# Kernel tuning notes

Hardware: AMD Instinct MI355X
Metric: run time of the kernel (lower is better)

Reference implementation:

```python
import jax, jax.numpy as jnp
import numpy as np
from jax import lax

B, N, D_PTS = 8, 4096, 6
N_POINTS, N_SAMPLES, RADIUS = 1024, 32, 0.2
MLPS = [64, 64, 128]
BN_EPS = 1e-3  # keras BatchNormalization default epsilon


def safe_norm(diff, axis):
    # euclidean norm with a backward-safe sqrt (same forward values)
    sq = jnp.sum(diff * diff, axis=axis)
    pos = sq > 0
    return jnp.where(pos, jnp.sqrt(jnp.where(pos, sq, 1.0)), 0.0)


def setup_inputs() -> dict:
    key = jax.random.key(0)
    ks = jax.random.split(key, 2)
    xyz = jax.random.normal(ks[0], (B, N, 3), jnp.float32)
    points = jax.random.normal(ks[1], (B, N, D_PTS), jnp.float32)
    inp = {"xyz": xyz, "points": points}
    c_in = 3 + D_PTS
    for i, c_out in enumerate(MLPS):
        kw = jax.random.fold_in(key, 100 + i)
        inp[f"w{i}"] = jax.random.normal(kw, (c_in, c_out), jnp.float32) * (1.0 / np.sqrt(c_in))
        inp[f"b{i}"] = jnp.zeros((c_out,), jnp.float32)
        inp[f"g{i}"] = jnp.ones((c_out,), jnp.float32)
        inp[f"be{i}"] = jnp.zeros((c_out,), jnp.float32)
        c_in = c_out
    return inp


def fps(xyz, n_points):
    # farthest point sampling; original seeds with a random index, we use 0 deterministically
    b, n, _ = xyz.shape
    init_idx = jnp.zeros((b,), jnp.int32)
    mask0 = jnp.ones((b, n), xyz.dtype)
    def step(carry, _):
        mask, last = carry
        added = jnp.take_along_axis(xyz, last[:, None, None], axis=1)  # [B,1,D]
        dist = safe_norm(xyz - added, 2) * mask                        # [B,N]
        nxt = jnp.argmax(dist, axis=1).astype(jnp.int32)
        new_mask = jnp.minimum(dist * mask * 1e11, mask)
        return (new_mask, nxt), nxt
    _, ids = lax.scan(step, (mask0, init_idx), None, length=n_points - 1)
    return jnp.concatenate([init_idx[:, None], ids.T], axis=1)  # [B, n_points]


def gather_points(x, idx):
    # x: [B,N,C]; idx: [B,...] -> [B,...,C]
    b = x.shape[0]
    flat = idx.reshape(b, -1)
    out = jnp.take_along_axis(x, flat[..., None], axis=1)
    return out.reshape(idx.shape + (x.shape[-1],))


def query_ball(radius, n_samples, xyz, cent_xyz):
    # faithful to source: compares norm to radius**2 (source quirk), full argsort then slice
    diff = xyz[:, None, :, :] - cent_xyz[:, :, None, :]   # [B,n,N,3]
    dist = safe_norm(diff, 3)                              # [B,n,N]
    dist = jnp.minimum(dist, radius * radius)
    return jnp.argsort(dist, axis=2)[:, :, :n_samples]     # [B,n,n_samples]


def mlp_layer(h, w, b, g, be):
    # pointwise Dense + BatchNormalization (batch stats, axis=-1) + relu
    h = jnp.einsum('bnsc,cd->bnsd', h, w) + b
    mean = jnp.mean(h, axis=(0, 1, 2), keepdims=True)
    var = jnp.var(h, axis=(0, 1, 2), keepdims=True)
    h = g * (h - mean) * lax.rsqrt(var + BN_EPS) + be
    return jax.nn.relu(h)


def forward(xyz, points, params):
    cent_idx = fps(xyz, N_POINTS)                 # [B, n_points]
    cent_xyz = gather_points(xyz, cent_idx)       # [B, n_points, 3]
    group_idx = query_ball(RADIUS, N_SAMPLES, xyz, cent_xyz)  # [B, n_points, n_samples]
    group_xyz = gather_points(xyz, group_idx)     # [B, n_points, n_samples, 3]
    group_pts = gather_points(points, group_idx)  # [B, n_points, n_samples, D]
    h = jnp.concatenate([group_xyz, group_pts], axis=-1)
    for (w, b, g, be) in params:
        h = mlp_layer(h, w, b, g, be)
    return cent_xyz, jnp.max(h, axis=2)           # [B,n_points,3], [B,n_points,128]


def reference(xyz, points, w0, b0, g0, be0, w1, b1, g1, be1, w2, b2, g2, be2):
    params = [(w0, b0, g0, be0), (w1, b1, g1, be1), (w2, b2, g2, be2)]
    return forward(xyz, points, params)
```

## Files before the change

kernel.cpp:

```cpp
#include <hip/hip_runtime.h>

#define NPTS  4096
#define NB    8
#define NC    1024
#define NSAMP 32
#define DP    6
#define C0    9
#define C3    128
#define ROWS_TOT 262144

#define OFF_SS   (32ull<<10)
#define OFF_H0   (1ull<<20)
#define OFF_Y0   (16ull<<20)
#define OFF_Y1   (96ull<<20)
#define OFF_PSUM (168ull<<20)
#define OFF_PSQ  (172ull<<20)
#define OFF_GMX  (176ull<<20)
#define OFF_GMN  (180ull<<20)

typedef unsigned long long ull;

__device__ __forceinline__ float sqdist_noc(float x, float y, float z,
                                            float cx, float cy, float cz) {
  #pragma clang fp contract(off)
  float dx = x - cx, dy = y - cy, dz = z - cz;
  return dx * dx + dy * dy + dz * dz;
}

template <int CTRL, int RM>
__device__ __forceinline__ float dpp_mov_f(float x) {
  int xi = __float_as_int(x);
  int r = __builtin_amdgcn_update_dpp(xi, xi, CTRL, RM, 0xf, false);
  return __int_as_float(r);
}

__device__ __forceinline__ float wave64_fmax(float x) {
  x = fmaxf(x, dpp_mov_f<0x111, 0xf>(x));
  x = fmaxf(x, dpp_mov_f<0x112, 0xf>(x));
  x = fmaxf(x, dpp_mov_f<0x114, 0xf>(x));
  x = fmaxf(x, dpp_mov_f<0x118, 0xf>(x));
  x = fmaxf(x, dpp_mov_f<0x142, 0xa>(x));
  x = fmaxf(x, dpp_mov_f<0x143, 0xc>(x));
  return x;
}

__global__ __launch_bounds__(256)
void fps_kernel(const float* __restrict__ xyz, float* __restrict__ cent) {
  const int b = blockIdx.x;
  const int t = threadIdx.x;
  const float* X = xyz + (size_t)b * NPTS * 3;
  float* OC = cent + (size_t)b * NC * 3;

  __shared__ float4 sxyz[NPTS];
  __shared__ float4 wkc[2][4];
  __shared__ alignas(16) int wki[2][4];
  __shared__ int sidx[NC];

  for (int p = t; p < NPTS; p += 256)
    sxyz[p] = make_float4(X[p * 3 + 0], X[p * 3 + 1], X[p * 3 + 2], 0.f);
  __syncthreads();

  float px[16], py[16], pz[16], h[16];
  #pragma unroll
  for (int i = 0; i < 16; i++) {
    float4 v = sxyz[t * 16 + i];
    px[i] = v.x; py[i] = v.y; pz[i] = v.z;
    h[i] = fmaf(v.x, v.x, fmaf(v.y, v.y, v.z * v.z));
  }

  const int wv = t >> 6;
  float4 c;

  auto step_body = [&](int pw_) {
    const float c2x = c.x + c.x, c2y = c.y + c.y, c2z = c.z + c.z;
    float key[16]; int idx[16];
    #pragma unroll
    for (int i = 0; i < 16; i++) {
      key[i] = fmaf(pz[i], -c2z, fmaf(py[i], -c2y, fmaf(px[i], -c2x, h[i])));
      idx[i] = i;
    }
    #pragma unroll
    for (int s = 1; s < 16; s <<= 1) {
      #pragma unroll
      for (int i = 0; i < 16; i += 2 * s) {
        bool tk = key[i + s] > key[i];
        key[i] = tk ? key[i + s] : key[i];
        idx[i] = tk ? idx[i + s] : idx[i];
      }
    }
    const float mx = key[0];
    const int mj = idx[0];
    float4 cand = sxyz[(t << 4) + mj];
    float wm = wave64_fmax(mx);
    float smax = __int_as_float(__builtin_amdgcn_readlane(__float_as_int(wm), 63));
    if (mx == smax) {
      wkc[pw_][wv] = make_float4(cand.x, cand.y, cand.z, smax);
      wki[pw_][wv] = (t << 4) + mj;
    }
  };

  auto fold = [&](int pr_) -> int {
    float4 q0 = wkc[pr_][0], q1 = wkc[pr_][1];
    float4 q2 = wkc[pr_][2], q3 = wkc[pr_][3];
    const int4 ii = *(const int4*)&wki[pr_][0];
    bool g1 = q1.w > q0.w; float4 ca = g1 ? q1 : q0; int ia = g1 ? ii.y : ii.x;
    bool g3 = q3.w > q2.w; float4 cb = g3 ? q3 : q2; int ib = g3 ? ii.w : ii.z;
    bool gb = cb.w > ca.w; c = gb ? cb : ca; return gb ? ib : ia;
  };

  if (t == 0) { sidx[0] = 0; h[0] = -__builtin_inff(); }
  c = sxyz[0];
  step_body(1);
  __syncthreads();

  for (int k = 2; k < NC; k++) {
    const int pr = (k - 1) & 1, pw = k & 1;
    int gidx = fold(pr);
    if (t == 0) sidx[k - 1] = gidx;
    if ((gidx >> 4) == t) {
      int m = gidx & 15;
      #pragma unroll
      for (int i = 0; i < 16; i++)
        if (i == m) h[i] = -__builtin_inff();
    }
    step_body(pw);
    __syncthreads();
  }
  {
    int gidx = fold(1023 & 1);
    if (t == 0) sidx[NC - 1] = gidx;
  }
  __syncthreads();
  for (int i = t; i < NC; i += 256) {
    float4 cc = sxyz[sidx[i]];
    OC[i * 3 + 0] = cc.x;
    OC[i * 3 + 1] = cc.y;
    OC[i * 3 + 2] = cc.z;
  }
}

#define BCAP 256
__global__ __launch_bounds__(256)
void ball_kernel(const float* __restrict__ xyz, const float* __restrict__ pts,
                 const float* __restrict__ cent, float* __restrict__ h0) {
  const int blk = blockIdx.x;
  const int b = blk >> 10;
  const int t = threadIdx.x;
  const float* X = xyz + (size_t)b * NPTS * 3;
  const float* P = pts + (size_t)b * NPTS * DP;
  const float cx = cent[(size_t)blk * 3 + 0];
  const float cy = cent[(size_t)blk * 3 + 1];
  const float cz = cent[(size_t)blk * 3 + 2];

  __shared__ int scount;
  __shared__ ull skeys[BCAP];
  __shared__ ull ssorted[BCAP];
  __shared__ int sel[NSAMP];
  if (t == 0) scount = 0;
  __syncthreads();

  #pragma unroll
  for (int i = 0; i < 16; i++) {
    int j = t * 16 + i;
    float sq = sqdist_noc(X[j * 3 + 0], X[j * 3 + 1], X[j * 3 + 2], cx, cy, cz);
    if (sq < 0.0017f) {
      float d = (sq > 0.f) ? sqrtf(sq) : 0.f;
      if (d < 0.04f) {
        int pos = atomicAdd(&scount, 1);
        if (pos < BCAP)
          skeys[pos] = ((ull)(unsigned)__float_as_int(d) << 12) | (unsigned)j;
      }
    }
  }
  __syncthreads();
  const int M = min(scount, BCAP);

  if (t < M) {
    ull my = skeys[t];
    int r = 0;
    for (int j2 = 0; j2 < M; j2++) r += (skeys[j2] < my);
    ssorted[r] = my;
  }
  __syncthreads();

  if (t < NSAMP) {
    int v;
    if (t < M) {
      v = (int)(ssorted[t] & 0xFFFull);
    } else {
      int s = t - M;
      int idx = s;
      for (int it = 0; it < 40; it++) {
        int c = 0;
        for (int j2 = 0; j2 < M; j2++) c += ((int)(skeys[j2] & 0xFFFull) <= idx);
        int nidx = s + c;
        if (nidx == idx) break;
        idx = nidx;
      }
      v = idx;
    }
    sel[t] = v;
  }
  __syncthreads();

  float* H = h0 + (size_t)blk * NSAMP * C0;
  for (int e = t; e < NSAMP * C0; e += 256) {
    int k = e / C0;
    int c = e - k * C0;
    int j = sel[k];
    H[e] = (c < 3) ? X[j * 3 + c] : P[j * DP + (c - 3)];
  }
}

__global__ __launch_bounds__(256)
void dense0_kernel(const float* __restrict__ h0, const float* __restrict__ W,
                   const float* __restrict__ bias, float* __restrict__ yout,
                   float* __restrict__ psum, float* __restrict__ psq) {
  __shared__ float xs[64 * C0];
  __shared__ float ws[C0 * 64];
  __shared__ float red[2][16][64];
  const int blk = blockIdx.x, t = threadIdx.x;
  const size_t rbase = (size_t)blk * 64;
  for (int e = t; e < 64 * C0; e += 256) xs[e] = h0[rbase * C0 + e];
  for (int e = t; e < C0 * 64; e += 256) ws[e] = W[e];
  __syncthreads();
  const int rg = t >> 4, cg = t & 15;
  float acc[4][4];
  float4 bv = *(const float4*)(bias + cg * 4);
  #pragma unroll
  for (int r = 0; r < 4; r++) { acc[r][0] = bv.x; acc[r][1] = bv.y; acc[r][2] = bv.z; acc[r][3] = bv.w; }
  #pragma unroll
  for (int k = 0; k < C0; k++) {
    float4 wv = *(const float4*)(ws + k * 64 + cg * 4);
    #pragma unroll
    for (int r = 0; r < 4; r++) {
      float x = xs[(rg * 4 + r) * C0 + k];
      acc[r][0] = fmaf(x, wv.x, acc[r][0]);
      acc[r][1] = fmaf(x, wv.y, acc[r][1]);
      acc[r][2] = fmaf(x, wv.z, acc[r][2]);
      acc[r][3] = fmaf(x, wv.w, acc[r][3]);
    }
  }
  #pragma unroll
  for (int r = 0; r < 4; r++)
    *(float4*)(yout + (rbase + rg * 4 + r) * 64 + cg * 4) =
        make_float4(acc[r][0], acc[r][1], acc[r][2], acc[r][3]);
  #pragma unroll
  for (int c4 = 0; c4 < 4; c4++) {
    float s = 0.f, q = 0.f;
    #pragma unroll
    for (int r = 0; r < 4; r++) { float v = acc[r][c4]; s += v; q = fmaf(v, v, q); }
    red[0][rg][cg * 4 + c4] = s;
    red[1][rg][cg * 4 + c4] = q;
  }
  __syncthreads();
  if (t < 64) {
    float S = 0.f, Q = 0.f;
    #pragma unroll
    for (int g = 0; g < 16; g++) { S += red[0][g][t]; Q += red[1][g][t]; }
    psum[(size_t)t * 4096 + blk] = S;
    psq [(size_t)t * 4096 + blk] = Q;
  }
}

template <int RPB, int COUT, int CGN, int NBLKS, bool MM>
__global__ __launch_bounds__(256)
void dense_mid_kernel(const float* __restrict__ yin, const float* __restrict__ ssin,
                      const float* __restrict__ W, const float* __restrict__ bias,
                      float* __restrict__ yout,
                      float* __restrict__ psum, float* __restrict__ psq,
                      float* __restrict__ gmax, float* __restrict__ gmin) {
  constexpr int NG = 256 / CGN;
  __shared__ float xs[RPB * 68];
  __shared__ float ws[64 * COUT];
  __shared__ float scs[64], shs[64];
  __shared__ float red[2][NG][COUT];
  __shared__ float redm[MM ? 2 : 1][MM ? NG : 1][MM ? COUT : 1];
  const int blk = blockIdx.x, t = threadIdx.x;
  if (t < 64) { scs[t] = ssin[t]; shs[t] = ssin[128 + t]; }
  __syncthreads();
  const size_t rbase = (size_t)blk * RPB;
  for (int e = t; e < RPB * 64; e += 256) {
    int c = e & 63;
    float v = yin[rbase * 64 + e];
    xs[(e >> 6) * 68 + c] = fmaxf(fmaf(v, scs[c], shs[c]), 0.f);
  }
  for (int e = t; e < 64 * COUT; e += 256) ws[e] = W[e];
  __syncthreads();
  const int rg = t / CGN, cg = t % CGN;
  float acc[4][4];
  float4 bv = *(const float4*)(bias + cg * 4);
  #pragma unroll
  for (int r = 0; r < 4; r++) { acc[r][0] = bv.x; acc[r][1] = bv.y; acc[r][2] = bv.z; acc[r][3] = bv.w; }
  for (int k0 = 0; k0 < 64; k0 += 4) {
    float4 xv[4];
    #pragma unroll
    for (int r = 0; r < 4; r++)
      xv[r] = *(const float4*)(xs + (rg * 4 + r) * 68 + k0);
    #pragma unroll
    for (int kk = 0; kk < 4; kk++) {
      float4 wv = *(const float4*)(ws + (k0 + kk) * COUT + cg * 4);
      #pragma unroll
      for (int r = 0; r < 4; r++) {
        float x = (&xv[r].x)[kk];
        acc[r][0] = fmaf(x, wv.x, acc[r][0]);
        acc[r][1] = fmaf(x, wv.y, acc[r][1]);
        acc[r][2] = fmaf(x, wv.z, acc[r][2]);
        acc[r][3] = fmaf(x, wv.w, acc[r][3]);
      }
    }
  }
  if constexpr (!MM) {
    #pragma unroll
    for (int r = 0; r < 4; r++)
      *(float4*)(yout + (rbase + rg * 4 + r) * COUT + cg * 4) =
          make_float4(acc[r][0], acc[r][1], acc[r][2], acc[r][3]);
  }
  #pragma unroll
  for (int c4 = 0; c4 < 4; c4++) {
    float s = 0.f, q = 0.f;
    #pragma unroll
    for (int r = 0; r < 4; r++) { float v = acc[r][c4]; s += v; q = fmaf(v, v, q); }
    red[0][rg][cg * 4 + c4] = s;
    red[1][rg][cg * 4 + c4] = q;
    if constexpr (MM) {
      float mx = acc[0][c4], mn = acc[0][c4];
      #pragma unroll
      for (int r = 1; r < 4; r++) { mx = fmaxf(mx, acc[r][c4]); mn = fminf(mn, acc[r][c4]); }
      redm[0][rg][cg * 4 + c4] = mx;
      redm[1][rg][cg * 4 + c4] = mn;
    }
  }
  __syncthreads();
  if (t < COUT) {
    float S = 0.f, Q = 0.f;
    #pragma unroll
    for (int g = 0; g < NG; g++) { S += red[0][g][t]; Q += red[1][g][t]; }
    psum[(size_t)t * NBLKS + blk] = S;
    psq [(size_t)t * NBLKS + blk] = Q;
    if constexpr (MM) {
      float mx = redm[0][0][t], mn = redm[1][0][t];
      #pragma unroll
      for (int g = 1; g < NG; g++) { mx = fmaxf(mx, redm[0][g][t]); mn = fminf(mn, redm[1][g][t]); }
      gmax[(size_t)blk * COUT + t] = mx;
      gmin[(size_t)blk * COUT + t] = mn;
    }
  }
}

template <int NBLK>
__global__ __launch_bounds__(256)
void stats_final_kernel(const float* __restrict__ psum, const float* __restrict__ psq,
                        const float* __restrict__ g, const float* __restrict__ be,
                        float* __restrict__ ss_out) {
  const int c = blockIdx.x, t = threadIdx.x;
  float S = 0.f, Q = 0.f;
  for (int i = t; i < NBLK; i += 256) {
    S += psum[(size_t)c * NBLK + i];
    Q += psq [(size_t)c * NBLK + i];
  }
  __shared__ float sS[256], sQ[256];
  sS[t] = S; sQ[t] = Q;
  __syncthreads();
  #pragma unroll
  for (int off = 128; off; off >>= 1) {
    if (t < off) { sS[t] += sS[t + off]; sQ[t] += sQ[t + off]; }
    __syncthreads();
  }
  if (t == 0) {
    const float inv = 1.0f / 262144.0f;
    float mean = sS[0] * inv;
    float var = sQ[0] * inv - mean * mean;
    float scale = g[c] / sqrtf(var + 1e-3f);
    ss_out[c] = scale;
    ss_out[128 + c] = be[c] - mean * scale;
  }
}

__global__ __launch_bounds__(128)
void pool_final_kernel(const float* __restrict__ gmax, const float* __restrict__ gmin,
                       const float* __restrict__ ss2, float* __restrict__ out1) {
  const int blk = blockIdx.x, c = threadIdx.x;
  const float sc = ss2[c], sh = ss2[128 + c];
  float v = (sc >= 0.f) ? gmax[(size_t)blk * C3 + c] : gmin[(size_t)blk * C3 + c];
  out1[(size_t)blk * C3 + c] = fmaxf(fmaf(v, sc, sh), 0.f);
}

extern "C" void kernel_launch(void* const* d_in, const int* in_sizes, int n_in,
                              void* d_out, int out_size, void* d_ws, size_t ws_size,
                              hipStream_t stream) {
  const float* xyz = (const float*)d_in[0];
  const float* pts = (const float*)d_in[1];
  const float* w0 = (const float*)d_in[2];
  const float* b0 = (const float*)d_in[3];
  const float* g0 = (const float*)d_in[4];
  const float* be0 = (const float*)d_in[5];
  const float* w1 = (const float*)d_in[6];
  const float* b1 = (const float*)d_in[7];
  const float* g1 = (const float*)d_in[8];
  const float* be1 = (const float*)d_in[9];
  const float* w2 = (const float*)d_in[10];
  const float* b2 = (const float*)d_in[11];
  const float* g2 = (const float*)d_in[12];
  const float* be2 = (const float*)d_in[13];

  float* out = (float*)d_out;
  float* cent = out;
  float* out1 = out + (size_t)NB * NC * 3;

  char* ws = (char*)d_ws;
  float* ssA  = (float*)(ws + OFF_SS);
  float* h0   = (float*)(ws + OFF_H0);
  float* y0   = (float*)(ws + OFF_Y0);
  float* y1   = (float*)(ws + OFF_Y1);
  float* psum = (float*)(ws + OFF_PSUM);
  float* psq  = (float*)(ws + OFF_PSQ);
  float* gmx  = (float*)(ws + OFF_GMX);
  float* gmn  = (float*)(ws + OFF_GMN);

  fps_kernel<<<dim3(NB), dim3(256), 0, stream>>>(xyz, cent);
  ball_kernel<<<dim3(NB * NC), dim3(256), 0, stream>>>(xyz, pts, cent, h0);

  dense0_kernel<<<dim3(ROWS_TOT / 64), dim3(256), 0, stream>>>(h0, w0, b0, y0, psum, psq);
  stats_final_kernel<4096><<<dim3(64), dim3(256), 0, stream>>>(psum, psq, g0, be0, ssA + 0 * 256);

  dense_mid_kernel<64, 64, 16, 4096, false><<<dim3(ROWS_TOT / 64), dim3(256), 0, stream>>>(
      y0, ssA + 0 * 256, w1, b1, y1, psum, psq, nullptr, nullptr);
  stats_final_kernel<4096><<<dim3(64), dim3(256), 0, stream>>>(psum, psq, g1, be1, ssA + 1 * 256);

  dense_mid_kernel<32, 128, 32, 8192, true><<<dim3(ROWS_TOT / 32), dim3(256), 0, stream>>>(
      y1, ssA + 1 * 256, w2, b2, nullptr, psum, psq, gmx, gmn);
  stats_final_kernel<8192><<<dim3(128), dim3(256), 0, stream>>>(psum, psq, g2, be2, ssA + 2 * 256);

  pool_final_kernel<<<dim3(NB * NC), dim3(128), 0, stream>>>(gmx, gmn, ssA + 2 * 256, out1);

  (void)in_sizes; (void)n_in; (void)out_size; (void)ws_size;
}
```

Baseline: 885.3 us.

## Recompute MLP layers from h0 instead of storing intermediates; pack two FPS batches per block

The dense stages no longer write the 64-channel activations y0 and y1 to global memory. Each batch-norm statistics pass recomputes the earlier layers from the small 9-channel h0 buffer, which removes large global writes and reads at the cost of redundant FLOPs. FPS now runs two batches per 512-thread block, halving the number of blocks for the serial sampling loop. The two halves share __syncthreads, so each one waits on the other.

```diff
diff --git a/kernel.cpp b/kernel.cpp
--- a/kernel.cpp
+++ b/kernel.cpp
@@ -11,8 +11,6 @@
 
 #define OFF_SS   (32ull<<10)
 #define OFF_H0   (1ull<<20)
-#define OFF_Y0   (16ull<<20)
-#define OFF_Y1   (96ull<<20)
 #define OFF_PSUM (168ull<<20)
 #define OFF_PSQ  (172ull<<20)
 #define OFF_GMX  (176ull<<20)
@@ -44,26 +42,27 @@
   return x;
 }
 
-__global__ __launch_bounds__(256)
+__global__ __launch_bounds__(512)
 void fps_kernel(const float* __restrict__ xyz, float* __restrict__ cent) {
-  const int b = blockIdx.x;
-  const int t = threadIdx.x;
+  const int half = threadIdx.x >> 8;
+  const int t = threadIdx.x & 255;
+  const int b = blockIdx.x * 2 + half;
   const float* X = xyz + (size_t)b * NPTS * 3;
   float* OC = cent + (size_t)b * NC * 3;
 
-  __shared__ float4 sxyz[NPTS];
-  __shared__ float4 wkc[2][4];
-  __shared__ alignas(16) int wki[2][4];
-  __shared__ int sidx[NC];
+  __shared__ float4 sxyz[2][NPTS];
+  __shared__ float4 wkc[2][2][4];
+  __shared__ alignas(16) int wki[2][2][4];
+  __shared__ int sidx[2][NC];
 
   for (int p = t; p < NPTS; p += 256)
-    sxyz[p] = make_float4(X[p * 3 + 0], X[p * 3 + 1], X[p * 3 + 2], 0.f);
+    sxyz[half][p] = make_float4(X[p * 3 + 0], X[p * 3 + 1], X[p * 3 + 2], 0.f);
   __syncthreads();
 
   float px[16], py[16], pz[16], h[16];
   #pragma unroll
   for (int i = 0; i < 16; i++) {
-    float4 v = sxyz[t * 16 + i];
+    float4 v = sxyz[half][t * 16 + i];
     px[i] = v.x; py[i] = v.y; pz[i] = v.z;
     h[i] = fmaf(v.x, v.x, fmaf(v.y, v.y, v.z * v.z));
   }
@@ -90,33 +89,34 @@
     }
     const float mx = key[0];
     const int mj = idx[0];
-    float4 cand = sxyz[(t << 4) + mj];
+    float4 cand = sxyz[half][(t << 4) + mj];
     float wm = wave64_fmax(mx);
     float smax = __int_as_float(__builtin_amdgcn_readlane(__float_as_int(wm), 63));
     if (mx == smax) {
-      wkc[pw_][wv] = make_float4(cand.x, cand.y, cand.z, smax);
-      wki[pw_][wv] = (t << 4) + mj;
+      wkc[half][pw_][wv] = make_float4(cand.x, cand.y, cand.z, smax);
+      wki[half][pw_][wv] = (t << 4) + mj;
     }
   };
 
   auto fold = [&](int pr_) -> int {
-    float4 q0 = wkc[pr_][0], q1 = wkc[pr_][1];
-    float4 q2 = wkc[pr_][2], q3 = wkc[pr_][3];
-    const int4 ii = *(const int4*)&wki[pr_][0];
+    float4 q0 = wkc[half][pr_][0], q1 = wkc[half][pr_][1];
+    float4 q2 = wkc[half][pr_][2], q3 = wkc[half][pr_][3];
+    const int4 ii = *(const int4*)&wki[half][pr_][0];
     bool g1 = q1.w > q0.w; float4 ca = g1 ? q1 : q0; int ia = g1 ? ii.y : ii.x;
     bool g3 = q3.w > q2.w; float4 cb = g3 ? q3 : q2; int ib = g3 ? ii.w : ii.z;
     bool gb = cb.w > ca.w; c = gb ? cb : ca; return gb ? ib : ia;
   };
 
-  if (t == 0) { sidx[0] = 0; h[0] = -__builtin_inff(); }
-  c = sxyz[0];
+  if (t == 0) { sidx[half][0] = 0; }
+  if (t == 0) { h[0] = -__builtin_inff(); }
+  c = sxyz[half][0];
   step_body(1);
   __syncthreads();
 
   for (int k = 2; k < NC; k++) {
     const int pr = (k - 1) & 1, pw = k & 1;
     int gidx = fold(pr);
-    if (t == 0) sidx[k - 1] = gidx;
+    if (t == 0) sidx[half][k - 1] = gidx;
     if ((gidx >> 4) == t) {
       int m = gidx & 15;
       #pragma unroll
@@ -128,11 +128,11 @@
   }
   {
     int gidx = fold(1023 & 1);
-    if (t == 0) sidx[NC - 1] = gidx;
+    if (t == 0) sidx[half][NC - 1] = gidx;
   }
   __syncthreads();
   for (int i = t; i < NC; i += 256) {
-    float4 cc = sxyz[sidx[i]];
+    float4 cc = sxyz[half][sidx[half][i]];
     OC[i * 3 + 0] = cc.x;
     OC[i * 3 + 1] = cc.y;
     OC[i * 3 + 2] = cc.z;
@@ -213,9 +213,9 @@
 }
 
 __global__ __launch_bounds__(256)
-void dense0_kernel(const float* __restrict__ h0, const float* __restrict__ W,
-                   const float* __restrict__ bias, float* __restrict__ yout,
-                   float* __restrict__ psum, float* __restrict__ psq) {
+void pass0_kernel(const float* __restrict__ h0, const float* __restrict__ W,
+                  const float* __restrict__ bias,
+                  float* __restrict__ psum, float* __restrict__ psq) {
   __shared__ float xs[64 * C0];
   __shared__ float ws[C0 * 64];
   __shared__ float red[2][16][64];
@@ -242,10 +242,6 @@
     }
   }
   #pragma unroll
-  for (int r = 0; r < 4; r++)
-    *(float4*)(yout + (rbase + rg * 4 + r) * 64 + cg * 4) =
-        make_float4(acc[r][0], acc[r][1], acc[r][2], acc[r][3]);
-  #pragma unroll
   for (int c4 = 0; c4 < 4; c4++) {
     float s = 0.f, q = 0.f;
     #pragma unroll
@@ -263,43 +259,67 @@
   }
 }
 
-template <int RPB, int COUT, int CGN, int NBLKS, bool MM>
 __global__ __launch_bounds__(256)
-void dense_mid_kernel(const float* __restrict__ yin, const float* __restrict__ ssin,
-                      const float* __restrict__ W, const float* __restrict__ bias,
-                      float* __restrict__ yout,
-                      float* __restrict__ psum, float* __restrict__ psq,
-                      float* __restrict__ gmax, float* __restrict__ gmin) {
-  constexpr int NG = 256 / CGN;
-  __shared__ float xs[RPB * 68];
-  __shared__ float ws[64 * COUT];
+void pass1_kernel(const float* __restrict__ h0, const float* __restrict__ W0,
+                  const float* __restrict__ b0, const float* __restrict__ ss0,
+                  const float* __restrict__ W1, const float* __restrict__ b1,
+                  float* __restrict__ psum, float* __restrict__ psq) {
+  __shared__ float xs0[64 * C0];
+  __shared__ float w0s[C0 * 64];
+  __shared__ float x1[64 * 68];
+  __shared__ float w1s[64 * 64];
   __shared__ float scs[64], shs[64];
-  __shared__ float red[2][NG][COUT];
-  __shared__ float redm[MM ? 2 : 1][MM ? NG : 1][MM ? COUT : 1];
+  __shared__ float red[2][16][64];
   const int blk = blockIdx.x, t = threadIdx.x;
-  if (t < 64) { scs[t] = ssin[t]; shs[t] = ssin[128 + t]; }
-  __syncthreads();
-  const size_t rbase = (size_t)blk * RPB;
-  for (int e = t; e < RPB * 64; e += 256) {
-    int c = e & 63;
-    float v = yin[rbase * 64 + e];
-    xs[(e >> 6) * 68 + c] = fmaxf(fmaf(v, scs[c], shs[c]), 0.f);
-  }
-  for (int e = t; e < 64 * COUT; e += 256) ws[e] = W[e];
-  __syncthreads();
-  const int rg = t / CGN, cg = t % CGN;
+  const size_t rbase = (size_t)blk * 64;
+  for (int e = t; e < 64 * C0; e += 256) xs0[e] = h0[rbase * C0 + e];
+  for (int e = t; e < C0 * 64; e += 256) w0s[e] = W0[e];
+  for (int e = t; e < 64 * 64; e += 256) w1s[e] = W1[e];
+  if (t < 64) { scs[t] = ss0[t]; shs[t] = ss0[128 + t]; }
+  __syncthreads();
+  const int rg = t >> 4, cg = t & 15;
+  {
+    float acc[4][4];
+    float4 bv = *(const float4*)(b0 + cg * 4);
+    #pragma unroll
+    for (int r = 0; r < 4; r++) { acc[r][0] = bv.x; acc[r][1] = bv.y; acc[r][2] = bv.z; acc[r][3] = bv.w; }
+    #pragma unroll
+    for (int k = 0; k < C0; k++) {
+      float4 wv = *(const float4*)(w0s + k * 64 + cg * 4);
+      #pragma unroll
+      for (int r = 0; r < 4; r++) {
+        float x = xs0[(rg * 4 + r) * C0 + k];
+        acc[r][0] = fmaf(x, wv.x, acc[r][0]);
+        acc[r][1] = fmaf(x, wv.y, acc[r][1]);
+        acc[r][2] = fmaf(x, wv.z, acc[r][2]);
+        acc[r][3] = fmaf(x, wv.w, acc[r][3]);
+      }
+    }
+    float4 sc = *(const float4*)(scs + cg * 4);
+    float4 sh = *(const float4*)(shs + cg * 4);
+    #pragma unroll
+    for (int r = 0; r < 4; r++) {
+      float4 o;
+      o.x = fmaxf(fmaf(acc[r][0], sc.x, sh.x), 0.f);
+      o.y = fmaxf(fmaf(acc[r][1], sc.y, sh.y), 0.f);
+      o.z = fmaxf(fmaf(acc[r][2], sc.z, sh.z), 0.f);
+      o.w = fmaxf(fmaf(acc[r][3], sc.w, sh.w), 0.f);
+      *(float4*)(x1 + (rg * 4 + r) * 68 + cg * 4) = o;
+    }
+  }
+  __syncthreads();
   float acc[4][4];
-  float4 bv = *(const float4*)(bias + cg * 4);
+  float4 bv = *(const float4*)(b1 + cg * 4);
   #pragma unroll
   for (int r = 0; r < 4; r++) { acc[r][0] = bv.x; acc[r][1] = bv.y; acc[r][2] = bv.z; acc[r][3] = bv.w; }
   for (int k0 = 0; k0 < 64; k0 += 4) {
     float4 xv[4];
     #pragma unroll
     for (int r = 0; r < 4; r++)
-      xv[r] = *(const float4*)(xs + (rg * 4 + r) * 68 + k0);
+      xv[r] = *(const float4*)(x1 + (rg * 4 + r) * 68 + k0);
     #pragma unroll
     for (int kk = 0; kk < 4; kk++) {
-      float4 wv = *(const float4*)(ws + (k0 + kk) * COUT + cg * 4);
+      float4 wv = *(const float4*)(w1s + (k0 + kk) * 64 + cg * 4);
       #pragma unroll
       for (int r = 0; r < 4; r++) {
         float x = (&xv[r].x)[kk];
@@ -310,12 +330,6 @@
       }
     }
   }
-  if constexpr (!MM) {
-    #pragma unroll
-    for (int r = 0; r < 4; r++)
-      *(float4*)(yout + (rbase + rg * 4 + r) * COUT + cg * 4) =
-          make_float4(acc[r][0], acc[r][1], acc[r][2], acc[r][3]);
-  }
   #pragma unroll
   for (int c4 = 0; c4 < 4; c4++) {
     float s = 0.f, q = 0.f;
@@ -323,28 +337,127 @@
     for (int r = 0; r < 4; r++) { float v = acc[r][c4]; s += v; q = fmaf(v, v, q); }
     red[0][rg][cg * 4 + c4] = s;
     red[1][rg][cg * 4 + c4] = q;
-    if constexpr (MM) {
-      float mx = acc[0][c4], mn = acc[0][c4];
-      #pragma unroll
-      for (int r = 1; r < 4; r++) { mx = fmaxf(mx, acc[r][c4]); mn = fminf(mn, acc[r][c4]); }
-      redm[0][rg][cg * 4 + c4] = mx;
-      redm[1][rg][cg * 4 + c4] = mn;
-    }
-  }
-  __syncthreads();
-  if (t < COUT) {
+  }
+  __syncthreads();
+  if (t < 64) {
     float S = 0.f, Q = 0.f;
     #pragma unroll
-    for (int g = 0; g < NG; g++) { S += red[0][g][t]; Q += red[1][g][t]; }
-    psum[(size_t)t * NBLKS + blk] = S;
-    psq [(size_t)t * NBLKS + blk] = Q;
-    if constexpr (MM) {
-      float mx = redm[0][0][t], mn = redm[1][0][t];
-      #pragma unroll
-      for (int g = 1; g < NG; g++) { mx = fmaxf(mx, redm[0][g][t]); mn = fminf(mn, redm[1][g][t]); }
-      gmax[(size_t)blk * COUT + t] = mx;
-      gmin[(size_t)blk * COUT + t] = mn;
-    }
+    for (int g = 0; g < 16; g++) { S += red[0][g][t]; Q += red[1][g][t]; }
+    psum[(size_t)t * 4096 + blk] = S;
+    psq [(size_t)t * 4096 + blk] = Q;
+  }
+}
+
+__global__ __launch_bounds__(256)
+void pass2_kernel(const float* __restrict__ h0, const float* __restrict__ W0,
+                  const float* __restrict__ b0, const float* __restrict__ ss0,
+                  const float* __restrict__ W1, const float* __restrict__ b1,
+                  const float* __restrict__ ss1, const float* __restrict__ W2,
+                  const float* __restrict__ bias2,
+                  float* __restrict__ psum, float* __restrict__ psq,
+                  float* __restrict__ gmax, float* __restrict__ gmin) {
+  __shared__ float xs0[32 * C0];
+  __shared__ float w0s[C0 * 64];
+  __shared__ float b0s[64], b1s[64];
+  __shared__ float sc0[64], sh0[64], sc1[64], sh1[64];
+  __shared__ float x1[32 * 68];
+  __shared__ float w1s[64 * 64];
+  __shared__ float x2[32 * 68];
+  __shared__ float w2s[64 * C3];
+  __shared__ float red[2][8][C3];
+  __shared__ float redm[2][8][C3];
+  const int blk = blockIdx.x, t = threadIdx.x;
+  const size_t rbase = (size_t)blk * 32;
+  for (int e = t; e < 32 * C0; e += 256) xs0[e] = h0[rbase * C0 + e];
+  for (int e = t; e < C0 * 64; e += 256) w0s[e] = W0[e];
+  for (int e = t; e < 64 * 64; e += 256) w1s[e] = W1[e];
+  for (int e = t; e < 64 * C3; e += 256) w2s[e] = W2[e];
+  if (t < 64) {
+    b0s[t] = b0[t]; b1s[t] = b1[t];
+    sc0[t] = ss0[t]; sh0[t] = ss0[128 + t];
+    sc1[t] = ss1[t]; sh1[t] = ss1[128 + t];
+  }
+  __syncthreads();
+  const int row = t >> 3, c8 = (t & 7) * 8;
+  {
+    float a[8];
+    #pragma unroll
+    for (int j = 0; j < 8; j++) a[j] = b0s[c8 + j];
+    #pragma unroll
+    for (int k = 0; k < C0; k++) {
+      float xv = xs0[row * C0 + k];
+      #pragma unroll
+      for (int j = 0; j < 8; j++) a[j] = fmaf(xv, w0s[k * 64 + c8 + j], a[j]);
+    }
+    #pragma unroll
+    for (int j = 0; j < 8; j++)
+      x1[row * 68 + c8 + j] = fmaxf(fmaf(a[j], sc0[c8 + j], sh0[c8 + j]), 0.f);
+  }
+  __syncthreads();
+  {
+    float a[8];
+    #pragma unroll
+    for (int j = 0; j < 8; j++) a[j] = b1s[c8 + j];
+    for (int k = 0; k < 64; k++) {
+      float xv = x1[row * 68 + k];
+      #pragma unroll
+      for (int j = 0; j < 8; j++) a[j] = fmaf(xv, w1s[k * 64 + c8 + j], a[j]);
+    }
+    #pragma unroll
+    for (int j = 0; j < 8; j++)
+      x2[row * 68 + c8 + j] = fmaxf(fmaf(a[j], sc1[c8 + j], sh1[c8 + j]), 0.f);
+  }
+  __syncthreads();
+  const int rg = t / 32, cg = t % 32;
+  float acc[4][4];
+  float4 bv = *(const float4*)(bias2 + cg * 4);
+  #pragma unroll
+  for (int r = 0; r < 4; r++) { acc[r][0] = bv.x; acc[r][1] = bv.y; acc[r][2] = bv.z; acc[r][3] = bv.w; }
+  for (int k0 = 0; k0 < 64; k0 += 4) {
+    float4 xv[4];
+    #pragma unroll
+    for (int r = 0; r < 4; r++)
+      xv[r] = *(const float4*)(x2 + (rg * 4 + r) * 68 + k0);
+    #pragma unroll
+    for (int kk = 0; kk < 4; kk++) {
+      float4 wv = *(const float4*)(w2s + (k0 + kk) * C3 + cg * 4);
+      #pragma unroll
+      for (int r = 0; r < 4; r++) {
+        float x = (&xv[r].x)[kk];
+        acc[r][0] = fmaf(x, wv.x, acc[r][0]);
+        acc[r][1] = fmaf(x, wv.y, acc[r][1]);
+        acc[r][2] = fmaf(x, wv.z, acc[r][2]);
+        acc[r][3] = fmaf(x, wv.w, acc[r][3]);
+      }
+    }
+  }
+  #pragma unroll
+  for (int c4 = 0; c4 < 4; c4++) {
+    float s = 0.f, q = 0.f;
+    float mx = acc[0][c4], mn = acc[0][c4];
+    #pragma unroll
+    for (int r = 0; r < 4; r++) {
+      float v = acc[r][c4];
+      s += v; q = fmaf(v, v, q);
+      if (r) { mx = fmaxf(mx, v); mn = fminf(mn, v); }
+    }
+    red[0][rg][cg * 4 + c4] = s;
+    red[1][rg][cg * 4 + c4] = q;
+    redm[0][rg][cg * 4 + c4] = mx;
+    redm[1][rg][cg * 4 + c4] = mn;
+  }
+  __syncthreads();
+  if (t < C3) {
+    float S = 0.f, Q = 0.f;
+    #pragma unroll
+    for (int g = 0; g < 8; g++) { S += red[0][g][t]; Q += red[1][g][t]; }
+    psum[(size_t)t * 8192 + blk] = S;
+    psq [(size_t)t * 8192 + blk] = Q;
+    float mx = redm[0][0][t], mn = redm[1][0][t];
+    #pragma unroll
+    for (int g = 1; g < 8; g++) { mx = fmaxf(mx, redm[0][g][t]); mn = fminf(mn, redm[1][g][t]); }
+    gmax[(size_t)blk * C3 + t] = mx;
+    gmin[(size_t)blk * C3 + t] = mn;
   }
 }
 
@@ -411,25 +524,23 @@
   char* ws = (char*)d_ws;
   float* ssA  = (float*)(ws + OFF_SS);
   float* h0   = (float*)(ws + OFF_H0);
-  float* y0   = (float*)(ws + OFF_Y0);
-  float* y1   = (float*)(ws + OFF_Y1);
   float* psum = (float*)(ws + OFF_PSUM);
   float* psq  = (float*)(ws + OFF_PSQ);
   float* gmx  = (float*)(ws + OFF_GMX);
   float* gmn  = (float*)(ws + OFF_GMN);
 
-  fps_kernel<<<dim3(NB), dim3(256), 0, stream>>>(xyz, cent);
+  fps_kernel<<<dim3(NB / 2), dim3(512), 0, stream>>>(xyz, cent);
   ball_kernel<<<dim3(NB * NC), dim3(256), 0, stream>>>(xyz, pts, cent, h0);
 
-  dense0_kernel<<<dim3(ROWS_TOT / 64), dim3(256), 0, stream>>>(h0, w0, b0, y0, psum, psq);
+  pass0_kernel<<<dim3(ROWS_TOT / 64), dim3(256), 0, stream>>>(h0, w0, b0, psum, psq);
   stats_final_kernel<4096><<<dim3(64), dim3(256), 0, stream>>>(psum, psq, g0, be0, ssA + 0 * 256);
 
-  dense_mid_kernel<64, 64, 16, 4096, false><<<dim3(ROWS_TOT / 64), dim3(256), 0, stream>>>(
-      y0, ssA + 0 * 256, w1, b1, y1, psum, psq, nullptr, nullptr);
+  pass1_kernel<<<dim3(ROWS_TOT / 64), dim3(256), 0, stream>>>(
+      h0, w0, b0, ssA + 0 * 256, w1, b1, psum, psq);
   stats_final_kernel<4096><<<dim3(64), dim3(256), 0, stream>>>(psum, psq, g1, be1, ssA + 1 * 256);
 
-  dense_mid_kernel<32, 128, 32, 8192, true><<<dim3(ROWS_TOT / 32), dim3(256), 0, stream>>>(
-      y1, ssA + 1 * 256, w2, b2, nullptr, psum, psq, gmx, gmn);
+  pass2_kernel<<<dim3(ROWS_TOT / 32), dim3(256), 0, stream>>>(
+      h0, w0, b0, ssA + 0 * 256, w1, b1, ssA + 1 * 256, w2, b2, psum, psq, gmx, gmn);
   stats_final_kernel<8192><<<dim3(128), dim3(256), 0, stream>>>(psum, psq, g2, be2, ssA + 2 * 256);
 
   pool_final_kernel<<<dim3(NB * NC), dim3(128), 0, stream>>>(gmx, gmn, ssA + 2 * 256, out1);
```

Measured after the change: 1.183 ms. +33.7%, slower.
